# Optimization experiments

Measured on AMD Instinct MI355X. Metric: run time of the kernel, lower is better.

Reference implementation:

```python
import jax, jax.numpy as jnp
import numpy as np

H = 1024      # hidden_size
I = 4096      # expert_intermediate_size (4*H)
E = 8         # num_experts (routed)
K = 2         # num_experts_per_token
SHARED = 1    # shared experts
LB_W = 0.01   # load_balance_loss_weight
Z_W = 0.01    # router z-loss weight
INIT_STD = 0.02


def _expert_mlp(x, gate_w, up_w, down_w):
    # SwiGLU expert: down( silu(x @ gate^T) * (x @ up^T) )
    return (jax.nn.silu(x @ gate_w.T) * (x @ up_w.T)) @ down_w.T


def setup_inputs() -> dict:
    key = jax.random.key(0)
    ks = jax.random.split(key, 8)
    f32 = jnp.float32
    return {
        'hidden_states': jax.random.normal(ks[0], (2, 2048, H), f32),
        'router_w': jax.random.normal(ks[1], (E, H), f32) * INIT_STD,
        'gate_w': jax.random.normal(ks[2], (E, I, H), f32) * INIT_STD,
        'up_w': jax.random.normal(ks[3], (E, I, H), f32) * INIT_STD,
        'down_w': jax.random.normal(ks[4], (E, H, I), f32) * INIT_STD,
        'sh_gate_w': jax.random.normal(ks[5], (I, H), f32) * INIT_STD,
        'sh_up_w': jax.random.normal(ks[6], (I, H), f32) * INIT_STD,
        'sh_down_w': jax.random.normal(ks[7], (H, I), f32) * INIT_STD,
    }


def reference(hidden_states, router_w, gate_w, up_w, down_w, sh_gate_w, sh_up_w, sh_down_w):
    B, S, Hd = hidden_states.shape
    x = hidden_states.reshape(-1, Hd)            # [T, H]
    T = x.shape[0]

    # Router (identity pre-router net, no bias)
    router_logits = x @ router_w.T               # [T, E]
    router_probs = jax.nn.softmax(router_logits, axis=-1)
    routing_weights, selected_experts = jax.lax.top_k(router_probs, K)  # [T, K]
    routing_weights = routing_weights / routing_weights.sum(-1, keepdims=True)

    # Per-token per-expert combine weights: sum_k w_k * [sel_k == e]
    onehot = jax.nn.one_hot(selected_experts, E, dtype=routing_weights.dtype)  # [T, K, E]
    combine = jnp.einsum('tk,tke->te', routing_weights, onehot)               # [T, E]

    # Routed experts (fixed small loop over E experts, vectorized over tokens)
    expert_out = jnp.zeros_like(x)
    for e in range(E):
        y = _expert_mlp(x, gate_w[e], up_w[e], down_w[e])                     # [T, H]
        expert_out = expert_out + y * combine[:, e:e + 1]

    # Shared expert(s) (SHARED == 1): averaged dense expert applied to all tokens
    shared_out = _expert_mlp(x, sh_gate_w, sh_up_w, sh_down_w) / SHARED

    final = (expert_out + shared_out).reshape(B, S, Hd)

    # Aux losses
    routed_mask = (onehot.sum(1) > 0).astype(jnp.float32)                     # [T, E]
    loads = jnp.concatenate([routed_mask.sum(0),
                             jnp.full((SHARED,), float(T), jnp.float32)])     # [E+SHARED]
    loads_n = loads / loads.sum()
    ideal = 1.0 / (E + SHARED)
    load_balance_loss = jnp.mean((loads_n - ideal) ** 2)
    router_z_loss = jnp.mean(jnp.sum(router_logits ** 2, axis=-1))
    total_aux_loss = LB_W * load_balance_loss + Z_W * router_z_loss
    return final, total_aux_loss
```

## Files before the change

### kernel.cpp

```cpp
#include <hip/hip_runtime.h>


typedef unsigned short u16;
typedef unsigned int u32;

typedef short bf16x8 __attribute__((ext_vector_type(8)));
typedef float f32x4 __attribute__((ext_vector_type(4)));

#define GLD16(g, l)                                                            \
  __builtin_amdgcn_global_load_lds(                                            \
      (const __attribute__((address_space(1))) void*)(g),                      \
      (__attribute__((address_space(3))) void*)(l), 16, 0, 0)

__device__ __forceinline__ u32 rne16(float f) {
  u32 u = __float_as_uint(f);
  return (u + 0x7fffu + ((u >> 16) & 1u)) >> 16;
}
__device__ __forceinline__ u16 bf16of(float f) { return (u16)rne16(f); }

__device__ __forceinline__ u32 cvt2(float lo, float hi) {
  u32 r;
  asm("v_cvt_pk_bf16_f32 %0, %1, %2" : "=v"(r) : "v"(lo), "v"(hi));
  return r;
}

__device__ __forceinline__ int xcd_remap_act(int lin, int nact) {
  int xcd = lin & 7, idx = lin >> 3;
  int q = nact >> 3, r = nact & 7;
  int base = xcd < r ? xcd * (q + 1) : r * (q + 1) + (xcd - r) * q;
  return base + idx;
}


__global__ void zero_meta_kernel(int* __restrict__ meta) {
  int t = threadIdx.x;
  if (t < 8) meta[t] = 0;
  if (t == 8) ((float*)(meta + 32))[0] = 0.0f;
}

__global__ void zero_out_kernel(float4* __restrict__ o) {
  o[blockIdx.x * 256 + threadIdx.x] = make_float4(0.f, 0.f, 0.f, 0.f);
}

__global__ void router_kernel(const float* __restrict__ x,
                              const float* __restrict__ rw,
                              u16* __restrict__ xb, int* __restrict__ tlist,
                              float* __restrict__ gwv, int* __restrict__ meta) {
  int tok = blockIdx.x;
  int lane = threadIdx.x;
  const float* xr = x + (size_t)tok * 1024;
  float acc[8] = {0.f, 0.f, 0.f, 0.f, 0.f, 0.f, 0.f, 0.f};
#pragma unroll
  for (int c = 0; c < 16; c++) {
    float xv = xr[lane + 64 * c];
    xb[(size_t)tok * 1024 + lane + 64 * c] = bf16of(xv);
#pragma unroll
    for (int e = 0; e < 8; e++) acc[e] += xv * rw[e * 1024 + lane + 64 * c];
  }
#pragma unroll
  for (int e = 0; e < 8; e++) {
    float v = acc[e];
    for (int m = 32; m > 0; m >>= 1) v += __shfl_xor(v, m, 64);
    acc[e] = v;
  }
  if (lane == 0) {
    float z = 0.f;
#pragma unroll
    for (int e = 0; e < 8; e++) z += acc[e] * acc[e];
    atomicAdd((float*)(meta + 32), z);
    int i1 = 0;
    float b1 = acc[0];
#pragma unroll
    for (int e = 1; e < 8; e++)
      if (acc[e] > b1) { b1 = acc[e]; i1 = e; }
    int i2 = -1;
    float b2 = -3.0e38f;
#pragma unroll
    for (int e = 0; e < 8; e++)
      if (e != i1 && acc[e] > b2) { b2 = acc[e]; i2 = e; }
    float w1 = 1.0f / (1.0f + __expf(b2 - b1));
    float w2 = 1.0f - w1;
    int s1 = atomicAdd(&meta[i1], 1);
    tlist[i1 * 4096 + s1] = tok;
    gwv[i1 * 4096 + s1] = w1;
    int s2 = atomicAdd(&meta[i2], 1);
    tlist[i2 * 4096 + s2] = tok;
    gwv[i2 * 4096 + s2] = w2;
  }
}

__global__ void finalize_kernel(int* __restrict__ meta, float* __restrict__ out) {
  if (threadIdx.x == 0) {
    int* basep = meta + 16;
    int base = 0;
    float lb = 0.f;
    const float invsum = 1.0f / 12288.0f;
    const float ideal = 1.0f / 9.0f;
    for (int e = 0; e < 8; e++) {
      int c = meta[e];
      int p = (c + 127) & ~127;
      basep[e] = base;
      base += p;
      float d = (float)c * invsum - ideal;
      lb += d * d;
    }
    basep[8] = base;
    basep[9] = base + 4096;
    meta[8] = 4096;
    float dsh = 4096.0f * invsum - ideal;
    lb += dsh * dsh;
    lb *= (1.0f / 9.0f);
    float z = ((float*)(meta + 32))[0] * (1.0f / 4096.0f);
    out[4194304] = 0.01f * lb + 0.01f * z;
  }
}

__global__ void gather_kernel(const u16* __restrict__ xb, u16* __restrict__ Ag,
                              const int* __restrict__ tlist,
                              const int* __restrict__ meta) {
  int r = blockIdx.x;
  int t = threadIdx.x;
  const int* base = meta + 16;
  int total = base[8];
  uint4 val = make_uint4(0u, 0u, 0u, 0u);
  if (r < total) {
    int e = 0;
#pragma unroll
    for (int q = 1; q < 8; q++)
      if (r >= base[q]) e = q;
    int s = r - base[e];
    if (s < meta[e]) {
      int tok = tlist[e * 4096 + s];
      val = *((const uint4*)(xb + (size_t)tok * 1024) + t);
    }
  }
  *((uint4*)(Ag + (size_t)r * 1024) + t) = val;
}

__global__ __launch_bounds__(256, 2) void gemm1_kernel(
    const u16* __restrict__ Ag, const u16* __restrict__ xb,
    const float* __restrict__ Wg, const float* __restrict__ Wu,
    const float* __restrict__ sg, const float* __restrict__ su,
    u16* __restrict__ Hout, const int* __restrict__ meta) {
  __shared__ u16 sA[128 * 32];
  __shared__ u16 sBg[128 * 32];
  __shared__ u16 sBu[128 * 32];

  const int* base = meta + 16;
  int gx = gridDim.x;
  int nby = base[9] >> 7;
  int nact = nby * gx;
  int lin = blockIdx.x + gx * blockIdx.y;
  if (lin >= nact) return;
  int wg = xcd_remap_act(lin, nact);
  int per = 8 * gx;
  int nfull = nby >> 3;
  int by, bx;
  if (wg < nfull * per) {
    int stripe = wg / per, ins = wg % per;
    by = stripe * 8 + (ins & 7);
    bx = ins >> 3;
  } else {
    int rem = wg - nfull * per;
    int sh = nby - nfull * 8;
    by = nfull * 8 + rem % sh;
    bx = rem / sh;
  }

  int r0 = by * 128;
  int e = 0;
#pragma unroll
  for (int q = 1; q <= 8; q++)
    if (r0 >= base[q]) e = q;

  const u16* Asrc =
      (e == 8) ? (xb + ((size_t)(r0 - base[8]) << 10)) : (Ag + ((size_t)r0 << 10));
  const float* gw = (e == 8) ? sg : (Wg + (size_t)e * 4194304);
  const float* uw = (e == 8) ? su : (Wu + (size_t)e * 4194304);

  int n0 = bx * 128;
  int t = threadIdx.x;
  int trow = t >> 2, tcol = (t & 3) * 8;

  const u16* aP = Asrc + (size_t)trow * 1024 + tcol;
  const float* gP = gw + (size_t)(n0 + trow) * 1024 + tcol;
  const float* uP = uw + (size_t)(n0 + trow) * 1024 + tcol;
  u16* aD = sA + t * 8;
  u16* gD = sBg + t * 8;
  u16* uD = sBu + t * 8;

  int lane = t & 63, wid = t >> 6;
  int wm = wid >> 1, wn = wid & 1;
  int l15 = lane & 15, quad = lane >> 4;
  const u16* aR = sA + (wm * 64 + l15) * 32 + quad * 8;
  const u16* gR = sBg + (wn * 64 + l15) * 32 + quad * 8;
  const u16* uR = sBu + (wn * 64 + l15) * 32 + quad * 8;

  f32x4 accg[4][4] = {};
  f32x4 accu[4][4] = {};

#pragma unroll 1
  for (int kk = 0; kk < 32; kk++) {
    if (kk) __syncthreads();
    GLD16(aP, aD);
    GLD16(aP + 65536, aD + 2048);
    float4 g0 = *(const float4*)gP;
    float4 g1 = *(const float4*)(gP + 4);
    float4 g2 = *(const float4*)(gP + 65536);
    float4 g3 = *(const float4*)(gP + 65540);
    float4 u0 = *(const float4*)uP;
    float4 u1 = *(const float4*)(uP + 4);
    float4 u2 = *(const float4*)(uP + 65536);
    float4 u3 = *(const float4*)(uP + 65540);
    uint4 w0, w1;
    w0.x = cvt2(g0.x, g0.y); w0.y = cvt2(g0.z, g0.w);
    w0.z = cvt2(g1.x, g1.y); w0.w = cvt2(g1.z, g1.w);
    w1.x = cvt2(g2.x, g2.y); w1.y = cvt2(g2.z, g2.w);
    w1.z = cvt2(g3.x, g3.y); w1.w = cvt2(g3.z, g3.w);
    *(uint4*)gD = w0;
    *(uint4*)(gD + 2048) = w1;
    w0.x = cvt2(u0.x, u0.y); w0.y = cvt2(u0.z, u0.w);
    w0.z = cvt2(u1.x, u1.y); w0.w = cvt2(u1.z, u1.w);
    w1.x = cvt2(u2.x, u2.y); w1.y = cvt2(u2.z, u2.w);
    w1.z = cvt2(u3.x, u3.y); w1.w = cvt2(u3.z, u3.w);
    *(uint4*)uD = w0;
    *(uint4*)(uD + 2048) = w1;
    aP += 32;
    gP += 32;
    uP += 32;
    __syncthreads();

    bf16x8 af[4];
#pragma unroll
    for (int i = 0; i < 4; i++) af[i] = *(const bf16x8*)(aR + i * 512);
#pragma unroll
    for (int j = 0; j < 4; j++) {
      bf16x8 bg = *(const bf16x8*)(gR + j * 512);
      bf16x8 bu = *(const bf16x8*)(uR + j * 512);
#pragma unroll
      for (int i = 0; i < 4; i++) {
        accg[i][j] =
            __builtin_amdgcn_mfma_f32_16x16x32_bf16(af[i], bg, accg[i][j], 0, 0, 0);
        accu[i][j] =
            __builtin_amdgcn_mfma_f32_16x16x32_bf16(af[i], bu, accu[i][j], 0, 0, 0);
      }
    }
  }

#pragma unroll
  for (int i = 0; i < 4; i++) {
    int row = r0 + wm * 64 + i * 16 + quad * 4;
#pragma unroll
    for (int r = 0; r < 4; r++) {
      u16* hrow = Hout + (size_t)(row + r) * 4096 + n0 + wn * 64 + l15;
#pragma unroll
      for (int j = 0; j < 4; j++) {
        float g = accg[i][j][r];
        float u = accu[i][j][r];
        float s = g / (1.0f + __expf(-g));
        hrow[j * 16] = bf16of(s * u);
      }
    }
  }
}

__global__ __launch_bounds__(256, 3) void gemm2_kernel(
    const u16* __restrict__ A, const float* __restrict__ Wd,
    const float* __restrict__ sd, float* __restrict__ out,
    const int* __restrict__ meta, const int* __restrict__ tlist,
    const float* __restrict__ gwv) {
  __shared__ u16 sA[128 * 32];
  __shared__ u16 sB[128 * 32];

  const int* base = meta + 16;
  int gx = gridDim.x;
  int nby = base[9] >> 7;
  int actz = nby * gx;
  int nact = actz * 2;
  int lin = blockIdx.x + gx * (blockIdx.y + gridDim.y * blockIdx.z);
  if (lin >= nact) return;
  int wg = xcd_remap_act(lin, nact);
  int bz = wg / actz;
  int w2 = wg - bz * actz;
  int per = 4 * gx;
  int nfull = nby >> 2;
  int by, bx;
  if (w2 < nfull * per) {
    int stripe = w2 / per, ins = w2 % per;
    by = stripe * 4 + (ins & 3);
    bx = ins >> 2;
  } else {
    int rem = w2 - nfull * per;
    int sh = nby - nfull * 4;
    by = nfull * 4 + rem % sh;
    bx = rem / sh;
  }

  int r0 = by * 128;
  int e = 0;
#pragma unroll
  for (int q = 1; q <= 8; q++)
    if (r0 >= base[q]) e = q;
  const float* dwp = (e == 8) ? sd : (Wd + (size_t)e * 4194304);

  int n0 = bx * 128;
  int k0 = bz * 2048;
  int t = threadIdx.x;
  int trow = t >> 2, tcol = (t & 3) * 8;

  const u16* aP = A + (size_t)(r0 + trow) * 4096 + k0 + tcol;
  const float* bP = dwp + (size_t)(n0 + trow) * 4096 + k0 + tcol;
  u16* aD = sA + t * 8;
  u16* bD = sB + t * 8;

  int lane = t & 63, wid = t >> 6;
  int wm = wid >> 1, wn = wid & 1;
  int l15 = lane & 15, quad = lane >> 4;
  const u16* aR = sA + (wm * 64 + l15) * 32 + quad * 8;
  const u16* bR = sB + (wn * 64 + l15) * 32 + quad * 8;

  f32x4 acc[4][4] = {};

#pragma unroll 1
  for (int kk = 0; kk < 64; kk++) {
    if (kk) __syncthreads();
    GLD16(aP, aD);
    GLD16(aP + 262144, aD + 2048);
    float4 c0 = *(const float4*)bP;
    float4 c1 = *(const float4*)(bP + 4);
    float4 c2 = *(const float4*)(bP + 262144);
    float4 c3 = *(const float4*)(bP + 262148);
    uint4 w0, w1;
    w0.x = cvt2(c0.x, c0.y); w0.y = cvt2(c0.z, c0.w);
    w0.z = cvt2(c1.x, c1.y); w0.w = cvt2(c1.z, c1.w);
    w1.x = cvt2(c2.x, c2.y); w1.y = cvt2(c2.z, c2.w);
    w1.z = cvt2(c3.x, c3.y); w1.w = cvt2(c3.z, c3.w);
    *(uint4*)bD = w0;
    *(uint4*)(bD + 2048) = w1;
    aP += 32;
    bP += 32;
    __syncthreads();

    bf16x8 af[4];
#pragma unroll
    for (int i = 0; i < 4; i++) af[i] = *(const bf16x8*)(aR + i * 512);
#pragma unroll
    for (int j = 0; j < 4; j++) {
      bf16x8 bb = *(const bf16x8*)(bR + j * 512);
#pragma unroll
      for (int i = 0; i < 4; i++)
        acc[i][j] =
            __builtin_amdgcn_mfma_f32_16x16x32_bf16(af[i], bb, acc[i][j], 0, 0, 0);
    }
  }

  int cnt_e = meta[e];
  int base_e = base[e];
#pragma unroll
  for (int i = 0; i < 4; i++) {
#pragma unroll
    for (int r = 0; r < 4; r++) {
      int s = r0 - base_e + wm * 64 + i * 16 + quad * 4 + r;
      if (s < cnt_e) {
        int tok;
        float w;
        if (e == 8) {
          tok = s;
          w = 1.0f;
        } else {
          tok = tlist[e * 4096 + s];
          w = gwv[e * 4096 + s];
        }
        float* orow = out + (size_t)tok * 1024 + n0 + wn * 64 + l15;
#pragma unroll
        for (int j = 0; j < 4; j++) unsafeAtomicAdd(orow + j * 16, w * acc[i][j][r]);
      }
    }
  }
}

extern "C" void kernel_launch(void* const* d_in, const int* in_sizes, int n_in,
                              void* d_out, int out_size, void* d_ws,
                              size_t ws_size, hipStream_t stream) {
  const float* x = (const float*)d_in[0];
  const float* rw = (const float*)d_in[1];
  const float* gw_ = (const float*)d_in[2];
  const float* uw_ = (const float*)d_in[3];
  const float* dw_ = (const float*)d_in[4];
  const float* sg = (const float*)d_in[5];
  const float* su = (const float*)d_in[6];
  const float* sd = (const float*)d_in[7];
  float* out = (float*)d_out;
  char* ws = (char*)d_ws;

  int* meta = (int*)(ws + 0);
  int* tlist = (int*)(ws + 256);
  float* gwv = (float*)(ws + 131328);
  u16* xb = (u16*)(ws + 262400);
  u16* Ag = (u16*)(ws + 8651008);
  u16* Hb = (u16*)(ws + 27525376);

  zero_meta_kernel<<<1, 64, 0, stream>>>(meta);
  router_kernel<<<4096, 64, 0, stream>>>(x, rw, xb, tlist, gwv, meta);
  finalize_kernel<<<1, 64, 0, stream>>>(meta, out);
  gather_kernel<<<9216, 128, 0, stream>>>(xb, Ag, tlist, meta);
  zero_out_kernel<<<4096, 256, 0, stream>>>((float4*)out);

  gemm1_kernel<<<dim3(32, 104), 256, 0, stream>>>(Ag, xb, gw_, uw_, sg, su, Hb,
                                                  meta);
  gemm2_kernel<<<dim3(8, 104, 2), 256, 0, stream>>>(Hb, dw_, sd, out, meta,
                                                    tlist, gwv);
}
```

Measured before the change: 1.088 ms.

## Double-buffer LDS tiles in both expert GEMMs to overlap loads with MFMA

Both GEMM kernels now keep two LDS buffers. Each step issues the next tile's global loads before running the MFMAs on the current buffer, then converts and stores the prefetched fp32 weights afterwards, so each K step needs one barrier instead of two. The aim is to hide global-load latency behind matrix math. Launch bounds occupancy hints are also raised (gemm1 2→3, gemm2 3→4), which adds register pressure alongside the doubled LDS footprint and the prefetch registers, and could cause spills.

```diff
diff --git a/kernel.cpp b/kernel.cpp
--- a/kernel.cpp
+++ b/kernel.cpp
@@ -137,14 +137,73 @@
   *((uint4*)(Ag + (size_t)r * 1024) + t) = val;
 }
 
-__global__ __launch_bounds__(256, 2) void gemm1_kernel(
+
+#define G1_STEP(RA, RG, RU, WA, WG, WU, LAST)                                  \
+  {                                                                            \
+    if (!(LAST)) {                                                             \
+      GLD16(aP, WA + t * 8);                                                   \
+      GLD16(aP + 65536, WA + t * 8 + 2048);                                    \
+      pg0 = *(const float4*)gP;                                                \
+      pg1 = *(const float4*)(gP + 4);                                          \
+      pg2 = *(const float4*)(gP + 65536);                                      \
+      pg3 = *(const float4*)(gP + 65540);                                      \
+      pu0 = *(const float4*)uP;                                                \
+      pu1 = *(const float4*)(uP + 4);                                          \
+      pu2 = *(const float4*)(uP + 65536);                                      \
+      pu3 = *(const float4*)(uP + 65540);                                      \
+      aP += 32;                                                                \
+      gP += 32;                                                                \
+      uP += 32;                                                                \
+    }                                                                          \
+    {                                                                          \
+      bf16x8 af[4];                                                            \
+      _Pragma("unroll") for (int i = 0; i < 4; i++) af[i] =                    \
+          *(const bf16x8*)(RA + aRo + i * 512);                                \
+      _Pragma("unroll") for (int j = 0; j < 4; j++) {                          \
+        bf16x8 bg = *(const bf16x8*)(RG + bRo + j * 512);                      \
+        bf16x8 bu = *(const bf16x8*)(RU + bRo + j * 512);                      \
+        _Pragma("unroll") for (int i = 0; i < 4; i++) {                        \
+          accg[i][j] = __builtin_amdgcn_mfma_f32_16x16x32_bf16(                \
+              af[i], bg, accg[i][j], 0, 0, 0);                                 \
+          accu[i][j] = __builtin_amdgcn_mfma_f32_16x16x32_bf16(                \
+              af[i], bu, accu[i][j], 0, 0, 0);                                 \
+        }                                                                      \
+      }                                                                        \
+    }                                                                          \
+    if (!(LAST)) {                                                             \
+      uint4 w0, w1;                                                            \
+      w0.x = cvt2(pg0.x, pg0.y);                                               \
+      w0.y = cvt2(pg0.z, pg0.w);                                               \
+      w0.z = cvt2(pg1.x, pg1.y);                                               \
+      w0.w = cvt2(pg1.z, pg1.w);                                               \
+      w1.x = cvt2(pg2.x, pg2.y);                                               \
+      w1.y = cvt2(pg2.z, pg2.w);                                               \
+      w1.z = cvt2(pg3.x, pg3.y);                                               \
+      w1.w = cvt2(pg3.z, pg3.w);                                               \
+      *(uint4*)(WG + t * 8) = w0;                                              \
+      *(uint4*)(WG + t * 8 + 2048) = w1;                                       \
+      w0.x = cvt2(pu0.x, pu0.y);                                               \
+      w0.y = cvt2(pu0.z, pu0.w);                                               \
+      w0.z = cvt2(pu1.x, pu1.y);                                               \
+      w0.w = cvt2(pu1.z, pu1.w);                                               \
+      w1.x = cvt2(pu2.x, pu2.y);                                               \
+      w1.y = cvt2(pu2.z, pu2.w);                                               \
+      w1.z = cvt2(pu3.x, pu3.y);                                               \
+      w1.w = cvt2(pu3.z, pu3.w);                                               \
+      *(uint4*)(WU + t * 8) = w0;                                              \
+      *(uint4*)(WU + t * 8 + 2048) = w1;                                       \
+    }                                                                          \
+    __syncthreads();                                                           \
+  }
+
+__global__ __launch_bounds__(256, 3) void gemm1_kernel(
     const u16* __restrict__ Ag, const u16* __restrict__ xb,
     const float* __restrict__ Wg, const float* __restrict__ Wu,
     const float* __restrict__ sg, const float* __restrict__ su,
     u16* __restrict__ Hout, const int* __restrict__ meta) {
-  __shared__ u16 sA[128 * 32];
-  __shared__ u16 sBg[128 * 32];
-  __shared__ u16 sBu[128 * 32];
+  __shared__ u16 sA0[4096], sA1[4096];
+  __shared__ u16 sBg0[4096], sBg1[4096];
+  __shared__ u16 sBu0[4096], sBu1[4096];
 
   const int* base = meta + 16;
   int gx = gridDim.x;
@@ -185,66 +244,59 @@
   const u16* aP = Asrc + (size_t)trow * 1024 + tcol;
   const float* gP = gw + (size_t)(n0 + trow) * 1024 + tcol;
   const float* uP = uw + (size_t)(n0 + trow) * 1024 + tcol;
-  u16* aD = sA + t * 8;
-  u16* gD = sBg + t * 8;
-  u16* uD = sBu + t * 8;
 
   int lane = t & 63, wid = t >> 6;
   int wm = wid >> 1, wn = wid & 1;
   int l15 = lane & 15, quad = lane >> 4;
-  const u16* aR = sA + (wm * 64 + l15) * 32 + quad * 8;
-  const u16* gR = sBg + (wn * 64 + l15) * 32 + quad * 8;
-  const u16* uR = sBu + (wn * 64 + l15) * 32 + quad * 8;
+  int aRo = (wm * 64 + l15) * 32 + quad * 8;
+  int bRo = (wn * 64 + l15) * 32 + quad * 8;
 
   f32x4 accg[4][4] = {};
   f32x4 accu[4][4] = {};
+  float4 pg0, pg1, pg2, pg3, pu0, pu1, pu2, pu3;
+
+  GLD16(aP, sA0 + t * 8);
+  GLD16(aP + 65536, sA0 + t * 8 + 2048);
+  pg0 = *(const float4*)gP;
+  pg1 = *(const float4*)(gP + 4);
+  pg2 = *(const float4*)(gP + 65536);
+  pg3 = *(const float4*)(gP + 65540);
+  pu0 = *(const float4*)uP;
+  pu1 = *(const float4*)(uP + 4);
+  pu2 = *(const float4*)(uP + 65536);
+  pu3 = *(const float4*)(uP + 65540);
+  aP += 32;
+  gP += 32;
+  uP += 32;
+  {
+    uint4 w0, w1;
+    w0.x = cvt2(pg0.x, pg0.y);
+    w0.y = cvt2(pg0.z, pg0.w);
+    w0.z = cvt2(pg1.x, pg1.y);
+    w0.w = cvt2(pg1.z, pg1.w);
+    w1.x = cvt2(pg2.x, pg2.y);
+    w1.y = cvt2(pg2.z, pg2.w);
+    w1.z = cvt2(pg3.x, pg3.y);
+    w1.w = cvt2(pg3.z, pg3.w);
+    *(uint4*)(sBg0 + t * 8) = w0;
+    *(uint4*)(sBg0 + t * 8 + 2048) = w1;
+    w0.x = cvt2(pu0.x, pu0.y);
+    w0.y = cvt2(pu0.z, pu0.w);
+    w0.z = cvt2(pu1.x, pu1.y);
+    w0.w = cvt2(pu1.z, pu1.w);
+    w1.x = cvt2(pu2.x, pu2.y);
+    w1.y = cvt2(pu2.z, pu2.w);
+    w1.z = cvt2(pu3.x, pu3.y);
+    w1.w = cvt2(pu3.z, pu3.w);
+    *(uint4*)(sBu0 + t * 8) = w0;
+    *(uint4*)(sBu0 + t * 8 + 2048) = w1;
+  }
+  __syncthreads();
 
 #pragma unroll 1
-  for (int kk = 0; kk < 32; kk++) {
-    if (kk) __syncthreads();
-    GLD16(aP, aD);
-    GLD16(aP + 65536, aD + 2048);
-    float4 g0 = *(const float4*)gP;
-    float4 g1 = *(const float4*)(gP + 4);
-    float4 g2 = *(const float4*)(gP + 65536);
-    float4 g3 = *(const float4*)(gP + 65540);
-    float4 u0 = *(const float4*)uP;
-    float4 u1 = *(const float4*)(uP + 4);
-    float4 u2 = *(const float4*)(uP + 65536);
-    float4 u3 = *(const float4*)(uP + 65540);
-    uint4 w0, w1;
-    w0.x = cvt2(g0.x, g0.y); w0.y = cvt2(g0.z, g0.w);
-    w0.z = cvt2(g1.x, g1.y); w0.w = cvt2(g1.z, g1.w);
-    w1.x = cvt2(g2.x, g2.y); w1.y = cvt2(g2.z, g2.w);
-    w1.z = cvt2(g3.x, g3.y); w1.w = cvt2(g3.z, g3.w);
-    *(uint4*)gD = w0;
-    *(uint4*)(gD + 2048) = w1;
-    w0.x = cvt2(u0.x, u0.y); w0.y = cvt2(u0.z, u0.w);
-    w0.z = cvt2(u1.x, u1.y); w0.w = cvt2(u1.z, u1.w);
-    w1.x = cvt2(u2.x, u2.y); w1.y = cvt2(u2.z, u2.w);
-    w1.z = cvt2(u3.x, u3.y); w1.w = cvt2(u3.z, u3.w);
-    *(uint4*)uD = w0;
-    *(uint4*)(uD + 2048) = w1;
-    aP += 32;
-    gP += 32;
-    uP += 32;
-    __syncthreads();
-
-    bf16x8 af[4];
-#pragma unroll
-    for (int i = 0; i < 4; i++) af[i] = *(const bf16x8*)(aR + i * 512);
-#pragma unroll
-    for (int j = 0; j < 4; j++) {
-      bf16x8 bg = *(const bf16x8*)(gR + j * 512);
-      bf16x8 bu = *(const bf16x8*)(uR + j * 512);
-#pragma unroll
-      for (int i = 0; i < 4; i++) {
-        accg[i][j] =
-            __builtin_amdgcn_mfma_f32_16x16x32_bf16(af[i], bg, accg[i][j], 0, 0, 0);
-        accu[i][j] =
-            __builtin_amdgcn_mfma_f32_16x16x32_bf16(af[i], bu, accu[i][j], 0, 0, 0);
-      }
-    }
+  for (int kk = 0; kk < 32; kk += 2) {
+    G1_STEP(sA0, sBg0, sBu0, sA1, sBg1, sBu1, 0);
+    G1_STEP(sA1, sBg1, sBu1, sA0, sBg0, sBu0, (kk + 2) == 32);
   }
 
 #pragma unroll
@@ -264,13 +316,53 @@
   }
 }
 
-__global__ __launch_bounds__(256, 3) void gemm2_kernel(
+
+#define G2_STEP(RA, RB, WA, WB, LAST)                                          \
+  {                                                                            \
+    if (!(LAST)) {                                                             \
+      GLD16(aP, WA + t * 8);                                                   \
+      GLD16(aP + 262144, WA + t * 8 + 2048);                                   \
+      pb0 = *(const float4*)bP;                                                \
+      pb1 = *(const float4*)(bP + 4);                                          \
+      pb2 = *(const float4*)(bP + 262144);                                     \
+      pb3 = *(const float4*)(bP + 262148);                                     \
+      aP += 32;                                                                \
+      bP += 32;                                                                \
+    }                                                                          \
+    {                                                                          \
+      bf16x8 af[4];                                                            \
+      _Pragma("unroll") for (int i = 0; i < 4; i++) af[i] =                    \
+          *(const bf16x8*)(RA + aRo + i * 512);                                \
+      _Pragma("unroll") for (int j = 0; j < 4; j++) {                          \
+        bf16x8 bb = *(const bf16x8*)(RB + bRo + j * 512);                      \
+        _Pragma("unroll") for (int i = 0; i < 4; i++) acc[i][j] =              \
+            __builtin_amdgcn_mfma_f32_16x16x32_bf16(af[i], bb, acc[i][j], 0,   \
+                                                    0, 0);                     \
+      }                                                                        \
+    }                                                                          \
+    if (!(LAST)) {                                                             \
+      uint4 w0, w1;                                                            \
+      w0.x = cvt2(pb0.x, pb0.y);                                               \
+      w0.y = cvt2(pb0.z, pb0.w);                                               \
+      w0.z = cvt2(pb1.x, pb1.y);                                               \
+      w0.w = cvt2(pb1.z, pb1.w);                                               \
+      w1.x = cvt2(pb2.x, pb2.y);                                               \
+      w1.y = cvt2(pb2.z, pb2.w);                                               \
+      w1.z = cvt2(pb3.x, pb3.y);                                               \
+      w1.w = cvt2(pb3.z, pb3.w);                                               \
+      *(uint4*)(WB + t * 8) = w0;                                              \
+      *(uint4*)(WB + t * 8 + 2048) = w1;                                       \
+    }                                                                          \
+    __syncthreads();                                                           \
+  }
+
+__global__ __launch_bounds__(256, 4) void gemm2_kernel(
     const u16* __restrict__ A, const float* __restrict__ Wd,
     const float* __restrict__ sd, float* __restrict__ out,
     const int* __restrict__ meta, const int* __restrict__ tlist,
     const float* __restrict__ gwv) {
-  __shared__ u16 sA[128 * 32];
-  __shared__ u16 sB[128 * 32];
+  __shared__ u16 sA0[4096], sA1[4096];
+  __shared__ u16 sB0[4096], sB1[4096];
 
   const int* base = meta + 16;
   int gx = gridDim.x;
@@ -310,48 +402,43 @@
 
   const u16* aP = A + (size_t)(r0 + trow) * 4096 + k0 + tcol;
   const float* bP = dwp + (size_t)(n0 + trow) * 4096 + k0 + tcol;
-  u16* aD = sA + t * 8;
-  u16* bD = sB + t * 8;
 
   int lane = t & 63, wid = t >> 6;
   int wm = wid >> 1, wn = wid & 1;
   int l15 = lane & 15, quad = lane >> 4;
-  const u16* aR = sA + (wm * 64 + l15) * 32 + quad * 8;
-  const u16* bR = sB + (wn * 64 + l15) * 32 + quad * 8;
+  int aRo = (wm * 64 + l15) * 32 + quad * 8;
+  int bRo = (wn * 64 + l15) * 32 + quad * 8;
 
   f32x4 acc[4][4] = {};
+  float4 pb0, pb1, pb2, pb3;
+
+  GLD16(aP, sA0 + t * 8);
+  GLD16(aP + 262144, sA0 + t * 8 + 2048);
+  pb0 = *(const float4*)bP;
+  pb1 = *(const float4*)(bP + 4);
+  pb2 = *(const float4*)(bP + 262144);
+  pb3 = *(const float4*)(bP + 262148);
+  aP += 32;
+  bP += 32;
+  {
+    uint4 w0, w1;
+    w0.x = cvt2(pb0.x, pb0.y);
+    w0.y = cvt2(pb0.z, pb0.w);
+    w0.z = cvt2(pb1.x, pb1.y);
+    w0.w = cvt2(pb1.z, pb1.w);
+    w1.x = cvt2(pb2.x, pb2.y);
+    w1.y = cvt2(pb2.z, pb2.w);
+    w1.z = cvt2(pb3.x, pb3.y);
+    w1.w = cvt2(pb3.z, pb3.w);
+    *(uint4*)(sB0 + t * 8) = w0;
+    *(uint4*)(sB0 + t * 8 + 2048) = w1;
+  }
+  __syncthreads();
 
 #pragma unroll 1
-  for (int kk = 0; kk < 64; kk++) {
-    if (kk) __syncthreads();
-    GLD16(aP, aD);
-    GLD16(aP + 262144, aD + 2048);
-    float4 c0 = *(const float4*)bP;
-    float4 c1 = *(const float4*)(bP + 4);
-    float4 c2 = *(const float4*)(bP + 262144);
-    float4 c3 = *(const float4*)(bP + 262148);
-    uint4 w0, w1;
-    w0.x = cvt2(c0.x, c0.y); w0.y = cvt2(c0.z, c0.w);
-    w0.z = cvt2(c1.x, c1.y); w0.w = cvt2(c1.z, c1.w);
-    w1.x = cvt2(c2.x, c2.y); w1.y = cvt2(c2.z, c2.w);
-    w1.z = cvt2(c3.x, c3.y); w1.w = cvt2(c3.z, c3.w);
-    *(uint4*)bD = w0;
-    *(uint4*)(bD + 2048) = w1;
-    aP += 32;
-    bP += 32;
-    __syncthreads();
-
-    bf16x8 af[4];
-#pragma unroll
-    for (int i = 0; i < 4; i++) af[i] = *(const bf16x8*)(aR + i * 512);
-#pragma unroll
-    for (int j = 0; j < 4; j++) {
-      bf16x8 bb = *(const bf16x8*)(bR + j * 512);
-#pragma unroll
-      for (int i = 0; i < 4; i++)
-        acc[i][j] =
-            __builtin_amdgcn_mfma_f32_16x16x32_bf16(af[i], bb, acc[i][j], 0, 0, 0);
-    }
+  for (int kk = 0; kk < 64; kk += 2) {
+    G2_STEP(sA0, sB0, sA1, sB1, 0);
+    G2_STEP(sA1, sB1, sA0, sB0, (kk + 2) == 64);
   }
 
   int cnt_e = meta[e];
```

Measured after the change: 1.929 ms. +77.3%, slower.
